# Performance work log

Measured on AMD Instinct MI355X. Metric: run time of the kernel, lower is better.

Reference implementation:

```python
import jax, jax.numpy as jnp
import numpy as np

V, D, L, H, T, F = 32000, 1024, 8, 16, 128, 2816
DH = D // H
ROPE_BASE = 10000.0
EPS = 1e-5


def rmsnorm(x, w):
    return x * jax.lax.rsqrt(jnp.mean(x * x, axis=-1, keepdims=True) + EPS) * w


def rope_tables():
    inv = 1.0 / (ROPE_BASE ** (jnp.arange(0, DH, 2, dtype=jnp.float32) / DH))
    ang = jnp.arange(T, dtype=jnp.float32)[:, None] * inv[None, :]  # [T, DH//2]
    cos = jnp.concatenate([jnp.cos(ang), jnp.cos(ang)], axis=-1)    # [T, DH]
    sin = jnp.concatenate([jnp.sin(ang), jnp.sin(ang)], axis=-1)
    return cos, sin


def rotate_half(x):
    a, b = jnp.split(x, 2, axis=-1)
    return jnp.concatenate([-b, a], axis=-1)


def setup_inputs():
    key = jax.random.key(0)
    ks = jax.random.split(key, 9)
    s = 0.02
    return {
        'input_ids': jax.random.randint(ks[0], (1, T), 0, V),
        'emb': jax.random.normal(ks[1], (V, D), jnp.float32) * s,
        'Wq': jax.random.normal(ks[2], (L, D, D), jnp.float32) * s,
        'Wk': jax.random.normal(ks[3], (L, D, D), jnp.float32) * s,
        'Wv': jax.random.normal(ks[4], (L, D, D), jnp.float32) * s,
        'Wo': jax.random.normal(ks[5], (L, D, D), jnp.float32) * s,
        'Wg': jax.random.normal(ks[6], (L, D, F), jnp.float32) * s,
        'Wu': jax.random.normal(ks[7], (L, D, F), jnp.float32) * s,
        'Wd': jax.random.normal(ks[8], (L, F, D), jnp.float32) * s,
        'attn_norm': jnp.ones((L, D), jnp.float32),
        'ffn_norm': jnp.ones((L, D), jnp.float32),
        'norm_out': jnp.ones((D,), jnp.float32),
    }


def reference(input_ids, emb, Wq, Wk, Wv, Wo, Wg, Wu, Wd, attn_norm, ffn_norm, norm_out):
    cos, sin = rope_tables()
    ids = input_ids.reshape(-1)          # batch=1, as in the torch loop
    xs_emb = emb[ids]                    # [T, D] per-token embeddings
    scale = 1.0 / np.sqrt(DH).astype(np.float32)
    pos = jnp.arange(T)

    def token_step(cache, inp):
        kc, vc = cache                   # each [L, T, H, DH] paged KV cache
        x, t = inp                       # x: [D], t: scalar position
        c_t, s_t = cos[t], sin[t]        # [DH]
        pos_mask = pos <= t              # causal validity over cache slots

        def layer_step(h, per_layer):
            wq, wk, wv, wo, wg, wu, wd, an, fn, kc_l, vc_l = per_layer
            hn = rmsnorm(h, an)
            q = (hn @ wq).reshape(H, DH)
            k = (hn @ wk).reshape(H, DH)
            v = (hn @ wv).reshape(H, DH)
            q = q * c_t + rotate_half(q) * s_t
            k = k * c_t + rotate_half(k) * s_t
            kc_l = jax.lax.dynamic_update_slice(kc_l, k[None], (t, 0, 0))
            vc_l = jax.lax.dynamic_update_slice(vc_l, v[None], (t, 0, 0))
            scores = jnp.einsum('hd,thd->ht', q, kc_l) * scale   # [H, T]
            scores = jnp.where(pos_mask[None, :], scores, -1e9)
            attn = jax.nn.softmax(scores, axis=-1)
            o = jnp.einsum('ht,thd->hd', attn, vc_l).reshape(D) @ wo
            h = h + o
            hn2 = rmsnorm(h, fn)
            h = h + (jax.nn.silu(hn2 @ wg) * (hn2 @ wu)) @ wd
            return h, (kc_l, vc_l)

        x_out, (kc, vc) = jax.lax.scan(
            layer_step, x,
            (Wq, Wk, Wv, Wo, Wg, Wu, Wd, attn_norm, ffn_norm, kc, vc))
        return (kc, vc), x_out

    cache0 = (jnp.zeros((L, T, H, DH), jnp.float32),
              jnp.zeros((L, T, H, DH), jnp.float32))
    _, xs_out = jax.lax.scan(token_step, cache0, (xs_emb, pos))
    x_last = rmsnorm(xs_out[-1], norm_out)
    logits = emb @ x_last                # tied lm_head: [V]
    return logits
```

## Files before the change

kernel.cpp:

```cpp
#include <hip/hip_runtime.h>
#include <hip/hip_bf16.h>
#include <math.h>

namespace {
constexpr int V = 32000, D = 1024, L = 8, H = 16, T = 128, F = 2816, DH = 64;
constexpr float EPS = 1e-5f;
constexpr float SCALE = 0.125f;
constexpr int QKVN = 3 * D;
constexpr int GUN  = 2 * F;
constexpr int NP_Q = 4;
constexpr int NP_O = 8;
constexpr int NP_G = 4;
constexpr int NP_D = 11;
}

typedef __attribute__((ext_vector_type(8))) short short8;
typedef __attribute__((ext_vector_type(4))) float f32x4;

__device__ __forceinline__ unsigned short f2bf(float x) {
    union { float f; unsigned u; } v; v.f = x;
    unsigned r = v.u + 0x7FFFu + ((v.u >> 16) & 1u);
    return (unsigned short)(r >> 16);
}

__global__ void embed_rope_kernel(const int* __restrict__ ids, const float* __restrict__ emb,
                                  float* __restrict__ X,
                                  float* __restrict__ cosT, float* __restrict__ sinT) {
    int t = blockIdx.x, tid = threadIdx.x;
    int id = ids[t];
    ((float4*)(X + (size_t)t * D))[tid] = ((const float4*)(emb + (size_t)id * D))[tid];
    if (tid < 32) {
        float inv = powf(10000.0f, -(2.0f * (float)tid) / (float)DH);
        float ang = (float)t * inv;
        cosT[t * 32 + tid] = cosf(ang);
        sinT[t * 32 + tid] = sinf(ang);
    }
}

template<int NP, bool BF16OUT>
__launch_bounds__(256)
__global__ void rmsnorm_sum_kernel(float* __restrict__ X, const float* __restrict__ P,
                                   const float* __restrict__ w, void* __restrict__ Y) {
    int t = blockIdx.x, tid = threadIdx.x;
    float4 xv = ((float4*)(X + (size_t)t * D))[tid];
    #pragma unroll
    for (int c = 0; c < NP; ++c) {
        float4 pv = ((const float4*)(P + ((size_t)c * T + t) * D))[tid];
        xv.x += pv.x; xv.y += pv.y; xv.z += pv.z; xv.w += pv.w;
    }
    if (NP) ((float4*)(X + (size_t)t * D))[tid] = xv;
    float s = xv.x * xv.x + xv.y * xv.y + xv.z * xv.z + xv.w * xv.w;
    for (int o = 32; o >= 1; o >>= 1) s += __shfl_xor(s, o);
    __shared__ float red[4];
    if ((tid & 63) == 0) red[tid >> 6] = s;
    __syncthreads();
    float tot = red[0] + red[1] + red[2] + red[3];
    float r = rsqrtf(tot / (float)D + EPS);
    float4 wv = ((const float4*)w)[tid];
    if (BF16OUT) {
        ushort4 y;
        y.x = f2bf(xv.x * r * wv.x); y.y = f2bf(xv.y * r * wv.y);
        y.z = f2bf(xv.z * r * wv.z); y.w = f2bf(xv.w * r * wv.w);
        ((ushort4*)((unsigned short*)Y + (size_t)t * D))[tid] = y;
    } else {
        float4 y;
        y.x = xv.x * r * wv.x; y.y = xv.y * r * wv.y;
        y.z = xv.z * r * wv.z; y.w = xv.w * r * wv.w;
        ((float4*)((float*)Y + (size_t)t * D))[tid] = y;
    }
}

template<int CH>
__launch_bounds__(512)
__global__ void gemm64_kernel(const unsigned short* __restrict__ A, int lda,
                              const float* __restrict__ W0, const float* __restrict__ W1,
                              const float* __restrict__ W2, int ldw,
                              float* __restrict__ out, int ldo, int zColOff,
                              size_t chunkStride) {
    constexpr int STAGES = CH / 128;
    constexpr int LSTR = 136;
    __shared__ unsigned short Bst[2][64 * LSTR];
    const float* W = blockIdx.z == 0 ? W0 : (blockIdx.z == 1 ? W1 : W2);
    const int tid = threadIdx.x;
    const int wave = tid >> 6, lane = tid & 63;
    const int cg = wave & 3, mh = wave >> 2;
    const int n0 = blockIdx.x * 64;
    const int k0 = blockIdx.y * CH;
    const int sc = tid & 63;
    const int so = tid >> 6;
    const float* wCol = W + (size_t)k0 * ldw + n0 + sc;
    unsigned short* wp = &Bst[0][sc * LSTR];
    const int lrow = lane & 15;
    const int lqo = lane >> 4;
    const unsigned short* aB = A + (size_t)(mh * 64 + lrow) * lda + k0 + lqo * 8;
    const unsigned short* bRd = &Bst[0][(cg * 16 + lrow) * LSTR + lqo * 8];
    f32x4 acc[4] = {};
    float pre[16];
    auto ldst = [&](int s) {
        #pragma unroll
        for (int p = 0; p < 2; ++p) {
            const float* src = wCol + (size_t)(s * 128 + (so * 2 + p) * 8) * ldw;
            #pragma unroll
            for (int j = 0; j < 8; ++j) pre[p * 8 + j] = src[(size_t)j * ldw];
        }
    };
    auto wrst = [&](int buf) {
        #pragma unroll
        for (int p = 0; p < 2; ++p) {
            short8 bv;
            #pragma unroll
            for (int j = 0; j < 8; ++j) bv[j] = (short)f2bf(pre[p * 8 + j]);
            *(short8*)(wp + buf * (64 * LSTR) + (so * 2 + p) * 8) = bv;
        }
    };
    ldst(0);
    wrst(0);
    __syncthreads();
    #pragma unroll
    for (int s = 0; s < STAGES; ++s) {
        if (s + 1 < STAGES) ldst(s + 1);
        const unsigned short* rd = bRd + (s & 1) * (64 * LSTR);
        #pragma unroll
        for (int ks = 0; ks < 4; ++ks) {
            short8 b = *(const short8*)(rd + ks * 32);
            #pragma unroll
            for (int mf = 0; mf < 4; ++mf) {
                short8 a = *(const short8*)(aB + (size_t)(mf * 16) * lda + s * 128 + ks * 32);
                acc[mf] = __builtin_amdgcn_mfma_f32_16x16x32_bf16(a, b, acc[mf], 0, 0, 0);
            }
        }
        if (s + 1 < STAGES) {
            __syncthreads();
            wrst((s + 1) & 1);
            __syncthreads();
        }
    }
    const int col = zColOff * blockIdx.z + n0 + cg * 16 + lrow;
    float* op = out + blockIdx.y * chunkStride;
    #pragma unroll
    for (int mf = 0; mf < 4; ++mf) {
        int r0 = mh * 64 + mf * 16 + lqo * 4;
        #pragma unroll
        for (int r = 0; r < 4; ++r)
            op[(size_t)(r0 + r) * ldo + col] = acc[mf][r];
    }
}

__launch_bounds__(256)
__global__ void rope_reduce_kernel(const float* __restrict__ P,
                                   const float* __restrict__ cosT, const float* __restrict__ sinT,
                                   float* __restrict__ Qr, float* __restrict__ Kr,
                                   float* __restrict__ Vr) {
    int t = blockIdx.x, tid = threadIdx.x;
    int d0 = tid * 4;
    float4 q = {0.f, 0.f, 0.f, 0.f}, k = q, v = q;
    #pragma unroll
    for (int c = 0; c < NP_Q; ++c) {
        const float* base = P + ((size_t)c * T + t) * QKVN;
        float4 a = ((const float4*)base)[tid];
        float4 b = ((const float4*)(base + D))[tid];
        float4 w = ((const float4*)(base + 2 * D))[tid];
        q.x += a.x; q.y += a.y; q.z += a.z; q.w += a.w;
        k.x += b.x; k.y += b.y; k.z += b.z; k.w += b.w;
        v.x += w.x; v.y += w.y; v.z += w.z; v.w += w.w;
    }
    float4 c4 = *(const float4*)(cosT + t * 32 + (d0 & 31));
    float4 s4 = *(const float4*)(sinT + t * 32 + (d0 & 31));
    float sgn = (d0 & 32) ? 1.f : -1.f;
    float4 qp, kp;
    qp.x = __shfl_xor(q.x, 8); qp.y = __shfl_xor(q.y, 8);
    qp.z = __shfl_xor(q.z, 8); qp.w = __shfl_xor(q.w, 8);
    kp.x = __shfl_xor(k.x, 8); kp.y = __shfl_xor(k.y, 8);
    kp.z = __shfl_xor(k.z, 8); kp.w = __shfl_xor(k.w, 8);
    float4 qo, ko;
    qo.x = q.x * c4.x + sgn * qp.x * s4.x; qo.y = q.y * c4.y + sgn * qp.y * s4.y;
    qo.z = q.z * c4.z + sgn * qp.z * s4.z; qo.w = q.w * c4.w + sgn * qp.w * s4.w;
    ko.x = k.x * c4.x + sgn * kp.x * s4.x; ko.y = k.y * c4.y + sgn * kp.y * s4.y;
    ko.z = k.z * c4.z + sgn * kp.z * s4.z; ko.w = k.w * c4.w + sgn * kp.w * s4.w;
    *(float4*)(Qr + (size_t)t * D + d0) = qo;
    *(float4*)(Kr + (size_t)t * D + d0) = ko;
    *(float4*)(Vr + (size_t)t * D + d0) = v;
}

__launch_bounds__(256)
__global__ void attn_kernel(const float* __restrict__ Q, const float* __restrict__ Kc,
                            const float* __restrict__ Vc, unsigned short* __restrict__ AO) {
    int t = blockIdx.x;
    int wave = threadIdx.x >> 6, lane = threadIdx.x & 63;
    int h = blockIdx.y * 4 + wave;
    __shared__ float qs[4][64];
    __shared__ float ps[4][128];
    float* q = qs[wave];
    float* p = ps[wave];
    q[lane] = Q[(size_t)t * D + h * DH + lane];
    __syncthreads();
    int j0 = lane, j1 = lane + 64;
    const float* kr0 = Kc + (size_t)j0 * D + h * DH;
    const float* kr1 = Kc + (size_t)j1 * D + h * DH;
    float s0 = 0.f, s1 = 0.f;
    #pragma unroll
    for (int d = 0; d < DH; ++d) {
        float qd = q[d];
        s0 = fmaf(qd, kr0[d], s0);
        s1 = fmaf(qd, kr1[d], s1);
    }
    s0 = (j0 <= t) ? s0 * SCALE : -1e30f;
    s1 = (j1 <= t) ? s1 * SCALE : -1e30f;
    float m = fmaxf(s0, s1);
    for (int o = 32; o >= 1; o >>= 1) m = fmaxf(m, __shfl_xor(m, o));
    float e0 = (j0 <= t) ? __expf(s0 - m) : 0.f;
    float e1 = (j1 <= t) ? __expf(s1 - m) : 0.f;
    float sum = e0 + e1;
    for (int o = 32; o >= 1; o >>= 1) sum += __shfl_xor(sum, o);
    float inv = 1.f / sum;
    p[j0] = e0 * inv;
    p[j1] = e1 * inv;
    __syncthreads();
    const float* vcol = Vc + h * DH + lane;
    float a0 = 0.f, a1 = 0.f, a2 = 0.f, a3 = 0.f;
    #pragma unroll
    for (int j = 0; j < T; j += 4) {
        a0 = fmaf(p[j],     vcol[(size_t)(j)     * D], a0);
        a1 = fmaf(p[j + 1], vcol[(size_t)(j + 1) * D], a1);
        a2 = fmaf(p[j + 2], vcol[(size_t)(j + 2) * D], a2);
        a3 = fmaf(p[j + 3], vcol[(size_t)(j + 3) * D], a3);
    }
    AO[(size_t)t * D + h * DH + lane] = f2bf((a0 + a1) + (a2 + a3));
}

__launch_bounds__(256)
__global__ void silu_reduce_kernel(const float* __restrict__ P,
                                   unsigned short* __restrict__ Gact) {
    int t = blockIdx.y;
    int f = blockIdx.x * 256 + threadIdx.x;
    float g = 0.f, u = 0.f;
    #pragma unroll
    for (int c = 0; c < NP_G; ++c) {
        const float* base = P + ((size_t)c * T + t) * GUN;
        g += base[f];
        u += base[F + f];
    }
    Gact[(size_t)t * F + f] = f2bf(g / (1.f + __expf(-g)) * u);
}

__global__ void logits_kernel(const float* __restrict__ emb, const float* __restrict__ xl,
                              float* __restrict__ out) {
    __shared__ float x[D];
    int tid = threadIdx.x;
    ((float4*)x)[tid] = ((const float4*)xl)[tid];
    __syncthreads();
    int row = blockIdx.x * 4 + (tid >> 6);
    int lane = tid & 63;
    const float4* e4 = (const float4*)(emb + (size_t)row * D);
    const float4* x4 = (const float4*)x;
    float s = 0.f;
    #pragma unroll
    for (int k = lane; k < D / 4; k += 64) {
        float4 ev = e4[k], xv = x4[k];
        s += ev.x * xv.x + ev.y * xv.y + ev.z * xv.z + ev.w * xv.w;
    }
    for (int o = 32; o >= 1; o >>= 1) s += __shfl_xor(s, o);
    if (lane == 0) out[row] = s;
}

extern "C" void kernel_launch(void* const* d_in, const int* in_sizes, int n_in,
                              void* d_out, int out_size, void* d_ws, size_t ws_size,
                              hipStream_t stream) {
    const int*   ids = (const int*)d_in[0];
    const float* emb = (const float*)d_in[1];
    const float* Wq  = (const float*)d_in[2];
    const float* Wk  = (const float*)d_in[3];
    const float* Wv  = (const float*)d_in[4];
    const float* Wo  = (const float*)d_in[5];
    const float* Wg  = (const float*)d_in[6];
    const float* Wu  = (const float*)d_in[7];
    const float* Wd  = (const float*)d_in[8];
    const float* attn_norm = (const float*)d_in[9];
    const float* ffn_norm  = (const float*)d_in[10];
    const float* norm_out  = (const float*)d_in[11];
    float* out = (float*)d_out;

    size_t off = 0;
    auto alloc = [&](size_t bytes) {
        void* p = (char*)d_ws + off;
        off += (bytes + 255) & ~(size_t)255;
        return p;
    };
    float*          X     = (float*)alloc((size_t)T * D * 4);
    float*          P0    = (float*)alloc((size_t)NP_Q * T * QKVN * 4);
    float*          P1    = (float*)alloc((size_t)NP_O * T * D * 4);
    float*          P2    = (float*)alloc((size_t)NP_D * T * D * 4);
    float*          P3    = (float*)alloc((size_t)NP_G * T * GUN * 4);
    float*          Qr    = (float*)alloc((size_t)T * D * 4);
    float*          Kr    = (float*)alloc((size_t)T * D * 4);
    float*          Vr    = (float*)alloc((size_t)T * D * 4);
    float*          cosT  = (float*)alloc((size_t)T * 32 * 4);
    float*          sinT  = (float*)alloc((size_t)T * 32 * 4);
    float*          xl    = (float*)alloc((size_t)D * 4);
    unsigned short* Hn_bf = (unsigned short*)alloc((size_t)T * D * 2);
    unsigned short* AO_bf = (unsigned short*)alloc((size_t)T * D * 2);
    unsigned short* Gact  = (unsigned short*)alloc((size_t)T * F * 2);
    (void)ws_size;

    embed_rope_kernel<<<T, 256, 0, stream>>>(ids, emb, X, cosT, sinT);

    for (int l = 0; l < L; ++l) {
        const float* wq = Wq + (size_t)l * D * D;
        const float* wk = Wk + (size_t)l * D * D;
        const float* wv = Wv + (size_t)l * D * D;
        const float* wo = Wo + (size_t)l * D * D;
        const float* wg = Wg + (size_t)l * D * F;
        const float* wu = Wu + (size_t)l * D * F;
        const float* wd = Wd + (size_t)l * F * D;

        if (l == 0)
            rmsnorm_sum_kernel<0, true><<<T, 256, 0, stream>>>(
                X, P2, attn_norm + (size_t)l * D, Hn_bf);
        else
            rmsnorm_sum_kernel<NP_D, true><<<T, 256, 0, stream>>>(
                X, P2, attn_norm + (size_t)l * D, Hn_bf);
        gemm64_kernel<256><<<dim3(D / 64, NP_Q, 3), 512, 0, stream>>>(
            Hn_bf, D, wq, wk, wv, D, P0, QKVN, D, (size_t)T * QKVN);
        rope_reduce_kernel<<<T, 256, 0, stream>>>(P0, cosT, sinT, Qr, Kr, Vr);
        attn_kernel<<<dim3(T, H / 4), 256, 0, stream>>>(Qr, Kr, Vr, AO_bf);
        gemm64_kernel<128><<<dim3(D / 64, NP_O, 1), 512, 0, stream>>>(
            AO_bf, D, wo, wo, wo, D, P1, D, 0, (size_t)T * D);
        rmsnorm_sum_kernel<NP_O, true><<<T, 256, 0, stream>>>(
            X, P1, ffn_norm + (size_t)l * D, Hn_bf);
        gemm64_kernel<256><<<dim3(F / 64, NP_G, 2), 512, 0, stream>>>(
            Hn_bf, D, wg, wu, wu, F, P3, GUN, F, (size_t)T * GUN);
        silu_reduce_kernel<<<dim3(F / 256, T), 256, 0, stream>>>(P3, Gact);
        gemm64_kernel<256><<<dim3(D / 64, NP_D, 1), 512, 0, stream>>>(
            Gact, F, wd, wd, wd, D, P2, D, 0, (size_t)T * D);
    }

    rmsnorm_sum_kernel<NP_D, false><<<1, 256, 0, stream>>>(
        X + (size_t)(T - 1) * D, P2 + (size_t)(T - 1) * D, norm_out, xl);
    logits_kernel<<<V / 4, 256, 0, stream>>>(emb, xl, out);
}
```

Before: 707.9 us.

## Fuse split-K reduction, RoPE and attention into one per-head LDS kernel

Replaces the separate rope_reduce and attention kernels with a single kernel per (query-half, head). It sums the split-K partials, applies RoPE to K/Q and stages K, V and Q in shared memory, then computes causal softmax and PV from LDS. The first half skips keys beyond row 64. This removes a kernel launch and the Qr/Kr/Vr global round-trip, plus the strided global K/V reads. The cost is a grid of only 32 blocks, which leaves most CUs idle, and the block for the second query half redundantly reduces all K/V rows.

```diff
diff --git a/kernel.cpp b/kernel.cpp
--- a/kernel.cpp
+++ b/kernel.cpp
@@ -146,86 +146,122 @@
     }
 }
 
-__launch_bounds__(256)
-__global__ void rope_reduce_kernel(const float* __restrict__ P,
-                                   const float* __restrict__ cosT, const float* __restrict__ sinT,
-                                   float* __restrict__ Qr, float* __restrict__ Kr,
-                                   float* __restrict__ Vr) {
-    int t = blockIdx.x, tid = threadIdx.x;
-    int d0 = tid * 4;
-    float4 q = {0.f, 0.f, 0.f, 0.f}, k = q, v = q;
-    #pragma unroll
-    for (int c = 0; c < NP_Q; ++c) {
-        const float* base = P + ((size_t)c * T + t) * QKVN;
-        float4 a = ((const float4*)base)[tid];
-        float4 b = ((const float4*)(base + D))[tid];
-        float4 w = ((const float4*)(base + 2 * D))[tid];
-        q.x += a.x; q.y += a.y; q.z += a.z; q.w += a.w;
-        k.x += b.x; k.y += b.y; k.z += b.z; k.w += b.w;
-        v.x += w.x; v.y += w.y; v.z += w.z; v.w += w.w;
-    }
-    float4 c4 = *(const float4*)(cosT + t * 32 + (d0 & 31));
-    float4 s4 = *(const float4*)(sinT + t * 32 + (d0 & 31));
-    float sgn = (d0 & 32) ? 1.f : -1.f;
-    float4 qp, kp;
-    qp.x = __shfl_xor(q.x, 8); qp.y = __shfl_xor(q.y, 8);
-    qp.z = __shfl_xor(q.z, 8); qp.w = __shfl_xor(q.w, 8);
-    kp.x = __shfl_xor(k.x, 8); kp.y = __shfl_xor(k.y, 8);
-    kp.z = __shfl_xor(k.z, 8); kp.w = __shfl_xor(k.w, 8);
-    float4 qo, ko;
-    qo.x = q.x * c4.x + sgn * qp.x * s4.x; qo.y = q.y * c4.y + sgn * qp.y * s4.y;
-    qo.z = q.z * c4.z + sgn * qp.z * s4.z; qo.w = q.w * c4.w + sgn * qp.w * s4.w;
-    ko.x = k.x * c4.x + sgn * kp.x * s4.x; ko.y = k.y * c4.y + sgn * kp.y * s4.y;
-    ko.z = k.z * c4.z + sgn * kp.z * s4.z; ko.w = k.w * c4.w + sgn * kp.w * s4.w;
-    *(float4*)(Qr + (size_t)t * D + d0) = qo;
-    *(float4*)(Kr + (size_t)t * D + d0) = ko;
-    *(float4*)(Vr + (size_t)t * D + d0) = v;
-}
-
-__launch_bounds__(256)
-__global__ void attn_kernel(const float* __restrict__ Q, const float* __restrict__ Kc,
-                            const float* __restrict__ Vc, unsigned short* __restrict__ AO) {
-    int t = blockIdx.x;
-    int wave = threadIdx.x >> 6, lane = threadIdx.x & 63;
-    int h = blockIdx.y * 4 + wave;
-    __shared__ float qs[4][64];
-    __shared__ float ps[4][128];
-    float* q = qs[wave];
-    float* p = ps[wave];
-    q[lane] = Q[(size_t)t * D + h * DH + lane];
+__launch_bounds__(512)
+__global__ void attn_fused_kernel(const float* __restrict__ P0,
+                                  const float* __restrict__ cosT,
+                                  const float* __restrict__ sinT,
+                                  unsigned short* __restrict__ AO) {
+    constexpr int KP = 68;
+    __shared__ float Ks[128][KP];
+    __shared__ float Vs[128][KP];
+    __shared__ float Qs[64][KP];
+    __shared__ float ps[8][128];
+    const int half = blockIdx.x;
+    const int h = blockIdx.y;
+    const int tid = threadIdx.x;
+    const int wave = tid >> 6, lane = tid & 63;
+    const int hoff = h * DH;
+    const int q0 = half * 64;
+    const int rows = half ? 128 : 64;
+
+    for (int it = 0; it < rows / 16; ++it) {
+        int idx = it * 512 + tid;
+        int j = idx >> 5, d = idx & 31;
+        float ka = 0.f, kb = 0.f;
+        #pragma unroll
+        for (int c = 0; c < NP_Q; ++c) {
+            const float* b = P0 + ((size_t)c * T + j) * QKVN + D + hoff;
+            ka += b[d]; kb += b[d + 32];
+        }
+        float cc = cosT[j * 32 + d], sn = sinT[j * 32 + d];
+        Ks[j][d] = ka * cc - kb * sn;
+        Ks[j][d + 32] = kb * cc + ka * sn;
+    }
+    for (int it = 0; it < rows / 32; ++it) {
+        int idx = it * 512 + tid;
+        int j = idx >> 4, d4 = idx & 15;
+        float4 v = {0.f, 0.f, 0.f, 0.f};
+        #pragma unroll
+        for (int c = 0; c < NP_Q; ++c) {
+            float4 pv = *(const float4*)(P0 + ((size_t)c * T + j) * QKVN + 2 * D + hoff + d4 * 4);
+            v.x += pv.x; v.y += pv.y; v.z += pv.z; v.w += pv.w;
+        }
+        *(float4*)&Vs[j][d4 * 4] = v;
+    }
+    for (int it = 0; it < 4; ++it) {
+        int idx = it * 512 + tid;
+        int tq = idx >> 5, d = idx & 31;
+        int t = q0 + tq;
+        float qa = 0.f, qb = 0.f;
+        #pragma unroll
+        for (int c = 0; c < NP_Q; ++c) {
+            const float* b = P0 + ((size_t)c * T + t) * QKVN + hoff;
+            qa += b[d]; qb += b[d + 32];
+        }
+        float cc = cosT[t * 32 + d], sn = sinT[t * 32 + d];
+        Qs[tq][d] = qa * cc - qb * sn;
+        Qs[tq][d + 32] = qb * cc + qa * sn;
+    }
     __syncthreads();
-    int j0 = lane, j1 = lane + 64;
-    const float* kr0 = Kc + (size_t)j0 * D + h * DH;
-    const float* kr1 = Kc + (size_t)j1 * D + h * DH;
-    float s0 = 0.f, s1 = 0.f;
-    #pragma unroll
-    for (int d = 0; d < DH; ++d) {
-        float qd = q[d];
-        s0 = fmaf(qd, kr0[d], s0);
-        s1 = fmaf(qd, kr1[d], s1);
-    }
-    s0 = (j0 <= t) ? s0 * SCALE : -1e30f;
-    s1 = (j1 <= t) ? s1 * SCALE : -1e30f;
-    float m = fmaxf(s0, s1);
-    for (int o = 32; o >= 1; o >>= 1) m = fmaxf(m, __shfl_xor(m, o));
-    float e0 = (j0 <= t) ? __expf(s0 - m) : 0.f;
-    float e1 = (j1 <= t) ? __expf(s1 - m) : 0.f;
-    float sum = e0 + e1;
-    for (int o = 32; o >= 1; o >>= 1) sum += __shfl_xor(sum, o);
-    float inv = 1.f / sum;
-    p[j0] = e0 * inv;
-    p[j1] = e1 * inv;
-    __syncthreads();
-    const float* vcol = Vc + h * DH + lane;
-    float a0 = 0.f, a1 = 0.f, a2 = 0.f, a3 = 0.f;
-    #pragma unroll
-    for (int j = 0; j < T; j += 4) {
-        a0 = fmaf(p[j],     vcol[(size_t)(j)     * D], a0);
-        a1 = fmaf(p[j + 1], vcol[(size_t)(j + 1) * D], a1);
-        a2 = fmaf(p[j + 2], vcol[(size_t)(j + 2) * D], a2);
-        a3 = fmaf(p[j + 3], vcol[(size_t)(j + 3) * D], a3);
-    }
-    AO[(size_t)t * D + h * DH + lane] = f2bf((a0 + a1) + (a2 + a3));
+
+    for (int qi = 0; qi < 8; ++qi) {
+        int tq = wave * 8 + qi;
+        int t = q0 + tq;
+        const float4* qrow = (const float4*)Qs[tq];
+        int j0 = lane;
+        float s0 = 0.f, s1 = 0.f;
+        const float4* k0 = (const float4*)Ks[j0];
+        #pragma unroll
+        for (int d4 = 0; d4 < 16; ++d4) {
+            float4 qv = qrow[d4], kv = k0[d4];
+            s0 += qv.x * kv.x + qv.y * kv.y + qv.z * kv.z + qv.w * kv.w;
+        }
+        if (half) {
+            const float4* k1 = (const float4*)Ks[lane + 64];
+            #pragma unroll
+            for (int d4 = 0; d4 < 16; ++d4) {
+                float4 qv = qrow[d4], kv = k1[d4];
+                s1 += qv.x * kv.x + qv.y * kv.y + qv.z * kv.z + qv.w * kv.w;
+            }
+        }
+        bool v0 = (j0 <= t), v1 = half && (lane + 64 <= t);
+        s0 = v0 ? s0 * SCALE : -1e30f;
+        s1 = v1 ? s1 * SCALE : -1e30f;
+        float m = fmaxf(s0, s1);
+        for (int o = 32; o >= 1; o >>= 1) m = fmaxf(m, __shfl_xor(m, o));
+        float e0 = v0 ? __expf(s0 - m) : 0.f;
+        float e1 = v1 ? __expf(s1 - m) : 0.f;
+        float sum = e0 + e1;
+        for (int o = 32; o >= 1; o >>= 1) sum += __shfl_xor(sum, o);
+        float inv = 1.f / sum;
+        ps[wave][j0] = e0 * inv;
+        if (half) ps[wave][lane + 64] = e1 * inv;
+        int jg = lane >> 4, d4 = lane & 15;
+        int jspan = rows >> 2;
+        float4 acc = {0.f, 0.f, 0.f, 0.f};
+        const float* pw = ps[wave];
+        for (int j = jg * jspan; j < (jg + 1) * jspan; ++j) {
+            float pj = pw[j];
+            float4 vv = *(const float4*)&Vs[j][d4 * 4];
+            acc.x = fmaf(pj, vv.x, acc.x);
+            acc.y = fmaf(pj, vv.y, acc.y);
+            acc.z = fmaf(pj, vv.z, acc.z);
+            acc.w = fmaf(pj, vv.w, acc.w);
+        }
+        #pragma unroll
+        for (int o = 16; o <= 32; o <<= 1) {
+            acc.x += __shfl_xor(acc.x, o);
+            acc.y += __shfl_xor(acc.y, o);
+            acc.z += __shfl_xor(acc.z, o);
+            acc.w += __shfl_xor(acc.w, o);
+        }
+        if (jg == 0) {
+            ushort4 y;
+            y.x = f2bf(acc.x); y.y = f2bf(acc.y);
+            y.z = f2bf(acc.z); y.w = f2bf(acc.w);
+            *(ushort4*)(AO + (size_t)t * D + hoff + d4 * 4) = y;
+        }
+    }
 }
 
 __launch_bounds__(256)
@@ -291,9 +327,6 @@
     float*          P1    = (float*)alloc((size_t)NP_O * T * D * 4);
     float*          P2    = (float*)alloc((size_t)NP_D * T * D * 4);
     float*          P3    = (float*)alloc((size_t)NP_G * T * GUN * 4);
-    float*          Qr    = (float*)alloc((size_t)T * D * 4);
-    float*          Kr    = (float*)alloc((size_t)T * D * 4);
-    float*          Vr    = (float*)alloc((size_t)T * D * 4);
     float*          cosT  = (float*)alloc((size_t)T * 32 * 4);
     float*          sinT  = (float*)alloc((size_t)T * 32 * 4);
     float*          xl    = (float*)alloc((size_t)D * 4);
@@ -321,8 +354,7 @@
                 X, P2, attn_norm + (size_t)l * D, Hn_bf);
         gemm64_kernel<256><<<dim3(D / 64, NP_Q, 3), 512, 0, stream>>>(
             Hn_bf, D, wq, wk, wv, D, P0, QKVN, D, (size_t)T * QKVN);
-        rope_reduce_kernel<<<T, 256, 0, stream>>>(P0, cosT, sinT, Qr, Kr, Vr);
-        attn_kernel<<<dim3(T, H / 4), 256, 0, stream>>>(Qr, Kr, Vr, AO_bf);
+        attn_fused_kernel<<<dim3(2, H), 512, 0, stream>>>(P0, cosT, sinT, AO_bf);
         gemm64_kernel<128><<<dim3(D / 64, NP_O, 1), 512, 0, stream>>>(
             AO_bf, D, wo, wo, wo, D, P1, D, 0, (size_t)T * D);
         rmsnorm_sum_kernel<NP_O, true><<<T, 256, 0, stream>>>(
```

New measurement: 783.6 us. +10.7%, slower.
